# Performance work log

Hardware: AMD Instinct MI355X
Metric: run time of the kernel (lower is better)

The kernel has to match this reference:

```python
import jax, jax.numpy as jnp
import numpy as np

N_NODES = 50000


def setup_inputs() -> dict:
    key = jax.random.key(0)
    ks = jax.random.split(key, 12)
    node_features = jax.random.normal(ks[0], (50000, 256), dtype=jnp.float32)
    hedge_features = jax.random.normal(ks[1], (25000, 128), dtype=jnp.float32)
    node_senders = jax.random.randint(ks[2], (800000,), 0, 50000, dtype=jnp.int32)
    node_receivers = jnp.sort(jax.random.randint(ks[3], (800000,), 0, 50000, dtype=jnp.int32))
    node_convolution = jax.random.uniform(ks[4], (800000, 1), dtype=jnp.float32)
    hedge2node_senders = jax.random.randint(ks[5], (400000,), 0, 25000, dtype=jnp.int32)
    hedge2node_receivers = jnp.sort(jax.random.randint(ks[6], (400000,), 0, 50000, dtype=jnp.int32))
    hedge2node_convolution = jax.random.uniform(ks[7], (400000, 1), dtype=jnp.float32)
    # Linear params (flax convention: y = x @ W + b, W is [in, out])
    W_msg = jax.random.normal(ks[8], (256, 256), dtype=jnp.float32) / np.sqrt(256.0)
    b_msg = jax.random.normal(ks[9], (256,), dtype=jnp.float32) * 0.01
    W_scale = jax.random.normal(ks[10], (128, 256), dtype=jnp.float32) / np.sqrt(128.0)
    b_scale = jax.random.normal(ks[11], (256,), dtype=jnp.float32) * 0.01
    return {
        "node_features": node_features,
        "hedge_features": hedge_features,
        "node_senders": node_senders,
        "node_receivers": node_receivers,
        "node_convolution": node_convolution,
        "hedge2node_senders": hedge2node_senders,
        "hedge2node_receivers": hedge2node_receivers,
        "hedge2node_convolution": hedge2node_convolution,
        "W_msg": W_msg,
        "b_msg": b_msg,
        "W_scale": W_scale,
        "b_scale": b_scale,
    }


def reference(node_features, hedge_features, node_senders, node_receivers,
              node_convolution, hedge2node_senders, hedge2node_receivers,
              hedge2node_convolution, W_msg, b_msg, W_scale, b_scale):
    # node -> node message pipeline: gather, Linear, per-edge scale, segment_sum
    sender_features = node_features[node_senders]                     # [E, Fin]
    messages = sender_features @ W_msg + b_msg                        # [E, Fout]
    scaled_messages = node_convolution * messages                     # [E, Fout]
    gathered_messages = jax.ops.segment_sum(
        scaled_messages, node_receivers, num_segments=N_NODES)        # [N, Fout]
    # hedge -> node scaling pipeline: gather, Linear, per-edge scale, segment_sum
    hedge_sender_features = hedge_features[hedge2node_senders]        # [E2, Fh]
    hedge_messages = hedge_sender_features @ W_scale + b_scale        # [E2, Fout]
    scaled_hedge_messages = hedge2node_convolution * hedge_messages   # [E2, Fout]
    gathered_scaling = jax.ops.segment_sum(
        scaled_hedge_messages, hedge2node_receivers, num_segments=N_NODES)  # [N, Fout]
    # Hadamard combine
    return gathered_scaling * gathered_messages
```

## Files before the change

kernel.cpp:

```cpp
#include <hip/hip_runtime.h>


typedef __attribute__((ext_vector_type(8))) short bf16x8;
typedef __attribute__((ext_vector_type(4))) float f32x4;

static __device__ __forceinline__ unsigned short f2bf(float f) {
  unsigned u = __float_as_uint(f);
  u += 0x7fff + ((u >> 16) & 1);
  return (unsigned short)(u >> 16);
}
static __device__ __forceinline__ float bf2f(unsigned short h) {
  return __uint_as_float((unsigned)h << 16);
}

__global__ __launch_bounds__(256) void cvt_bf16(
    const float* __restrict__ src, unsigned short* __restrict__ dst, int n4)
{
  const int i = blockIdx.x * blockDim.x + threadIdx.x;
  if (i >= n4) return;
  const float4 v = reinterpret_cast<const float4*>(src)[i];
  reinterpret_cast<ushort4*>(dst)[i] =
      make_ushort4(f2bf(v.x), f2bf(v.y), f2bf(v.z), f2bf(v.w));
}

__global__ __launch_bounds__(256) void build_row_offsets(
    const int* __restrict__ rcv, int E, int N, int* __restrict__ row_start)
{
  const int e = blockIdx.x * blockDim.x + threadIdx.x;
  if (e >= E) return;
  const int c = rcv[e];
  const int p = (e == 0) ? -1 : rcv[e - 1];
  for (int n = p + 1; n <= c; ++n) row_start[n] = e;
  if (e == E - 1) {
    for (int n = c + 1; n <= N; ++n) row_start[n] = E;
  }
}

__global__ __launch_bounds__(256) void transpose_to_bf16(
    const float* __restrict__ W, unsigned short* __restrict__ WT, int K, int N)
{
  __shared__ float t[32][33];
  const int tx = threadIdx.x & 31, ty = threadIdx.x >> 5;
  const int n0 = blockIdx.x * 32, k0 = blockIdx.y * 32;
#pragma unroll
  for (int i = 0; i < 32; i += 8)
    t[ty + i][tx] = W[(size_t)(k0 + ty + i) * N + n0 + tx];
  __syncthreads();
#pragma unroll
  for (int i = 0; i < 32; i += 8)
    WT[(size_t)(n0 + ty + i) * K + k0 + tx] = f2bf(t[tx][ty + i]);
}

__global__ __launch_bounds__(256) void scatter_node_seg(
    const unsigned short* __restrict__ X,
    const int* __restrict__ snd,
    const float* __restrict__ conv,
    const int* __restrict__ row_start,
    unsigned short* __restrict__ A,
    float* __restrict__ csum,
    int N)
{
  const int lane = threadIdx.x & 63;
  const int node = __builtin_amdgcn_readfirstlane(
      (int)blockIdx.x * 4 + ((int)threadIdx.x >> 6));
  if (node >= N) return;
  const int lo = row_start[node];
  const int hi = row_start[node + 1];

  const unsigned short* Xl = X + lane * 4;
  float4 acc = make_float4(0.f, 0.f, 0.f, 0.f);
  float cacc = 0.f;

  int e = lo;
  for (; e + 8 <= hi; e += 8) {
    int s[8]; float cv[8]; ushort4 x[8];
#pragma unroll
    for (int j = 0; j < 8; ++j) s[j] = snd[e + j];
#pragma unroll
    for (int j = 0; j < 8; ++j) cv[j] = conv[e + j];
#pragma unroll
    for (int j = 0; j < 8; ++j)
      x[j] = *reinterpret_cast<const ushort4*>(Xl + (size_t)s[j] * 256);
#pragma unroll
    for (int j = 0; j < 8; ++j) {
      acc.x = fmaf(cv[j], bf2f(x[j].x), acc.x);
      acc.y = fmaf(cv[j], bf2f(x[j].y), acc.y);
      acc.z = fmaf(cv[j], bf2f(x[j].z), acc.z);
      acc.w = fmaf(cv[j], bf2f(x[j].w), acc.w);
      cacc += cv[j];
    }
  }
  for (; e < hi; ++e) {
    const int s = snd[e];
    const float cv = conv[e];
    const ushort4 x = *reinterpret_cast<const ushort4*>(Xl + (size_t)s * 256);
    acc.x = fmaf(cv, bf2f(x.x), acc.x);
    acc.y = fmaf(cv, bf2f(x.y), acc.y);
    acc.z = fmaf(cv, bf2f(x.z), acc.z);
    acc.w = fmaf(cv, bf2f(x.w), acc.w);
    cacc += cv;
  }

  *reinterpret_cast<ushort4*>(A + (size_t)node * 256 + lane * 4) =
      make_ushort4(f2bf(acc.x), f2bf(acc.y), f2bf(acc.z), f2bf(acc.w));
  if (lane == 0) csum[node] = cacc;
}

__global__ __launch_bounds__(256) void scatter_hedge_seg(
    const unsigned short* __restrict__ X,
    const int* __restrict__ snd,
    const float* __restrict__ conv,
    const int* __restrict__ row_start,
    unsigned short* __restrict__ B,
    float* __restrict__ csum,
    int N)
{
  const int lane = threadIdx.x & 63;
  const int node = __builtin_amdgcn_readfirstlane(
      (int)blockIdx.x * 4 + ((int)threadIdx.x >> 6));
  if (node >= N) return;
  const int lo = row_start[node];
  const int hi = row_start[node + 1];

  const unsigned short* Xl = X + lane * 2;
  float2 acc = make_float2(0.f, 0.f);
  float cacc = 0.f;

  int e = lo;
  for (; e + 8 <= hi; e += 8) {
    int s[8]; float cv[8]; ushort2 x[8];
#pragma unroll
    for (int j = 0; j < 8; ++j) s[j] = snd[e + j];
#pragma unroll
    for (int j = 0; j < 8; ++j) cv[j] = conv[e + j];
#pragma unroll
    for (int j = 0; j < 8; ++j)
      x[j] = *reinterpret_cast<const ushort2*>(Xl + (size_t)s[j] * 128);
#pragma unroll
    for (int j = 0; j < 8; ++j) {
      acc.x = fmaf(cv[j], bf2f(x[j].x), acc.x);
      acc.y = fmaf(cv[j], bf2f(x[j].y), acc.y);
      cacc += cv[j];
    }
  }
  for (; e < hi; ++e) {
    const int s = snd[e];
    const float cv = conv[e];
    const ushort2 x = *reinterpret_cast<const ushort2*>(Xl + (size_t)s * 128);
    acc.x = fmaf(cv, bf2f(x.x), acc.x);
    acc.y = fmaf(cv, bf2f(x.y), acc.y);
    cacc += cv;
  }

  *reinterpret_cast<ushort2*>(B + (size_t)node * 128 + lane * 2) =
      make_ushort2(f2bf(acc.x), f2bf(acc.y));
  if (lane == 0) csum[node] = cacc;
}

__global__ __launch_bounds__(512) void gemm_combine_mfma(
    const unsigned short* __restrict__ A,
    const unsigned short* __restrict__ B,
    const float* __restrict__ c1,
    const float* __restrict__ c2,
    const unsigned short* __restrict__ WmT,
    const float* __restrict__ bm,
    const unsigned short* __restrict__ WsT,
    const float* __restrict__ bs,
    float* __restrict__ out,
    int M)
{
  __shared__ unsigned short lWm[64][264];
  __shared__ unsigned short lWs[64][136];

  const int tid  = (int)threadIdx.x;
  const int lane = tid & 63;
  const int wv   = tid >> 6;
  const int l15  = lane & 15;
  const int lg   = lane >> 4;
  const int m0      = blockIdx.x * 256;
  const int colBlk  = blockIdx.y * 64;

  for (int i = tid; i < 64 * 256 / 8; i += 512) {
    const int c = i >> 5, k8 = (i & 31) << 3;
    *reinterpret_cast<bf16x8*>(&lWm[c][k8]) =
        *reinterpret_cast<const bf16x8*>(WmT + (size_t)(colBlk + c) * 256 + k8);
  }
  for (int i = tid; i < 64 * 128 / 8; i += 512) {
    const int c = i >> 4, k8 = (i & 15) << 3;
    *reinterpret_cast<bf16x8*>(&lWs[c][k8]) =
        *reinterpret_cast<const bf16x8*>(WsT + (size_t)(colBlk + c) * 128 + k8);
  }
  __syncthreads();

  const int rowA = m0 + wv * 32 + l15;

  f32x4 accM[2][4];
  f32x4 accS[2][4];
#pragma unroll
  for (int ms = 0; ms < 2; ++ms)
#pragma unroll
    for (int n = 0; n < 4; ++n) {
      accM[ms][n] = (f32x4)0.f;
      accS[ms][n] = (f32x4)0.f;
    }

#pragma unroll
  for (int kc = 0; kc < 256; kc += 32) {
    const int ko = kc + lg * 8;
    const bf16x8 a0 = *reinterpret_cast<const bf16x8*>(A + (size_t)rowA * 256 + ko);
    const bf16x8 a1 = *reinterpret_cast<const bf16x8*>(A + (size_t)(rowA + 16) * 256 + ko);
#pragma unroll
    for (int n = 0; n < 4; ++n) {
      const bf16x8 w = *reinterpret_cast<const bf16x8*>(&lWm[l15 + n * 16][ko]);
      accM[0][n] = __builtin_amdgcn_mfma_f32_16x16x32_bf16(a0, w, accM[0][n], 0, 0, 0);
      accM[1][n] = __builtin_amdgcn_mfma_f32_16x16x32_bf16(a1, w, accM[1][n], 0, 0, 0);
    }
  }

#pragma unroll
  for (int kc = 0; kc < 128; kc += 32) {
    const int ko = kc + lg * 8;
    const bf16x8 b0 = *reinterpret_cast<const bf16x8*>(B + (size_t)rowA * 128 + ko);
    const bf16x8 b1 = *reinterpret_cast<const bf16x8*>(B + (size_t)(rowA + 16) * 128 + ko);
#pragma unroll
    for (int n = 0; n < 4; ++n) {
      const bf16x8 w = *reinterpret_cast<const bf16x8*>(&lWs[l15 + n * 16][ko]);
      accS[0][n] = __builtin_amdgcn_mfma_f32_16x16x32_bf16(b0, w, accS[0][n], 0, 0, 0);
      accS[1][n] = __builtin_amdgcn_mfma_f32_16x16x32_bf16(b1, w, accS[1][n], 0, 0, 0);
    }
  }

  float bmv[4], bsv[4];
#pragma unroll
  for (int n = 0; n < 4; ++n) {
    bmv[n] = bm[colBlk + n * 16 + l15];
    bsv[n] = bs[colBlk + n * 16 + l15];
  }
#pragma unroll
  for (int ms = 0; ms < 2; ++ms) {
    const int rbase = m0 + wv * 32 + ms * 16 + lg * 4;
#pragma unroll
    for (int r = 0; r < 4; ++r) {
      const int row = rbase + r;
      if (row < M) {
        const float k1 = c1[row];
        const float k2 = c2[row];
#pragma unroll
        for (int n = 0; n < 4; ++n) {
          const int col = colBlk + n * 16 + l15;
          const float mv = accM[ms][n][r] + k1 * bmv[n];
          const float sv = accS[ms][n][r] + k2 * bsv[n];
          out[(size_t)row * 256 + col] = mv * sv;
        }
      }
    }
  }
}

extern "C" void kernel_launch(void* const* d_in, const int* in_sizes, int n_in,
                              void* d_out, int out_size, void* d_ws, size_t ws_size,
                              hipStream_t stream) {
  const float* node_features  = (const float*)d_in[0];
  const float* hedge_features = (const float*)d_in[1];
  const int*   node_senders   = (const int*)d_in[2];
  const int*   node_receivers = (const int*)d_in[3];
  const float* node_conv      = (const float*)d_in[4];
  const int*   h2n_senders    = (const int*)d_in[5];
  const int*   h2n_receivers  = (const int*)d_in[6];
  const float* h2n_conv       = (const float*)d_in[7];
  const float* Wm             = (const float*)d_in[8];
  const float* bm             = (const float*)d_in[9];
  const float* Ws             = (const float*)d_in[10];
  const float* bs             = (const float*)d_in[11];
  float* out = (float*)d_out;

  const int M   = in_sizes[0] / 256;
  const int Nh  = in_sizes[1] / 128;
  const int E   = in_sizes[2];
  const int E2  = in_sizes[5];
  const int Mp  = ((M + 255) / 256) * 256;

  unsigned short* Ab  = (unsigned short*)d_ws;
  unsigned short* Bb  = Ab + (size_t)Mp * 256;
  unsigned short* Xb  = Bb + (size_t)Mp * 128;
  unsigned short* Hb  = Xb + (size_t)M * 256;
  unsigned short* WmT = Hb + (size_t)Nh * 128;
  unsigned short* WsT = WmT + 256 * 256;
  float* c1 = (float*)(WsT + 256 * 128);
  float* c2 = c1 + Mp;
  int*   ro1 = (int*)(c2 + Mp);
  int*   ro2 = ro1 + (M + 1);

  const int nx4 = M * 256 / 4, nh4 = Nh * 128 / 4;
  cvt_bf16<<<(nx4 + 255) / 256, 256, 0, stream>>>(node_features, Xb, nx4);
  cvt_bf16<<<(nh4 + 255) / 256, 256, 0, stream>>>(hedge_features, Hb, nh4);

  build_row_offsets<<<(E + 255) / 256, 256, 0, stream>>>(
      node_receivers, E, M, ro1);
  build_row_offsets<<<(E2 + 255) / 256, 256, 0, stream>>>(
      h2n_receivers, E2, M, ro2);

  transpose_to_bf16<<<dim3(256 / 32, 256 / 32), 256, 0, stream>>>(
      Wm, WmT, 256, 256);
  transpose_to_bf16<<<dim3(256 / 32, 128 / 32), 256, 0, stream>>>(
      Ws, WsT, 128, 256);

  scatter_node_seg<<<(M + 3) / 4, 256, 0, stream>>>(
      Xb, node_senders, node_conv, ro1, Ab, c1, M);
  scatter_hedge_seg<<<(M + 3) / 4, 256, 0, stream>>>(
      Hb, h2n_senders, h2n_conv, ro2, Bb, c2, M);

  gemm_combine_mfma<<<dim3(Mp / 256, 4), 512, 0, stream>>>(
      Ab, Bb, c1, c2, WmT, bm, WsT, bs, out, M);
}
```

Before: 145.0 us.

## Merge prep kernels into one launch and fuse both segment scatters

The six preprocessing launches (bf16 conversions, row-offset builds, weight transposes) become a single kernel that dispatches on block index. The node and hedge segment-gather kernels are likewise merged into one grid, so both can run at the same time. The node path's unroll goes from 8 to 16 edges, with a 4-wide middle loop. The aim is to cut per-launch overhead and tail idle time between small kernels, at the cost of more register pressure in the fused gather kernel.

```diff
diff --git a/kernel.cpp b/kernel.cpp
--- a/kernel.cpp
+++ b/kernel.cpp
@@ -13,148 +13,209 @@
   return __uint_as_float((unsigned)h << 16);
 }
 
-__global__ __launch_bounds__(256) void cvt_bf16(
-    const float* __restrict__ src, unsigned short* __restrict__ dst, int n4)
-{
-  const int i = blockIdx.x * blockDim.x + threadIdx.x;
-  if (i >= n4) return;
-  const float4 v = reinterpret_cast<const float4*>(src)[i];
-  reinterpret_cast<ushort4*>(dst)[i] =
-      make_ushort4(f2bf(v.x), f2bf(v.y), f2bf(v.z), f2bf(v.w));
-}
-
-__global__ __launch_bounds__(256) void build_row_offsets(
-    const int* __restrict__ rcv, int E, int N, int* __restrict__ row_start)
-{
-  const int e = blockIdx.x * blockDim.x + threadIdx.x;
-  if (e >= E) return;
-  const int c = rcv[e];
-  const int p = (e == 0) ? -1 : rcv[e - 1];
-  for (int n = p + 1; n <= c; ++n) row_start[n] = e;
-  if (e == E - 1) {
-    for (int n = c + 1; n <= N; ++n) row_start[n] = E;
-  }
-}
-
-__global__ __launch_bounds__(256) void transpose_to_bf16(
-    const float* __restrict__ W, unsigned short* __restrict__ WT, int K, int N)
+__global__ __launch_bounds__(256) void prep_all(
+    const float* __restrict__ X, const float* __restrict__ H,
+    const int* __restrict__ rcv1, int E1,
+    const int* __restrict__ rcv2, int E2, int N,
+    const float* __restrict__ Wm, const float* __restrict__ Ws,
+    unsigned short* __restrict__ Xb, unsigned short* __restrict__ Hb,
+    int* __restrict__ ro1, int* __restrict__ ro2,
+    unsigned short* __restrict__ WmT, unsigned short* __restrict__ WsT,
+    int nX4, int nH4)
 {
   __shared__ float t[32][33];
-  const int tx = threadIdx.x & 31, ty = threadIdx.x >> 5;
-  const int n0 = blockIdx.x * 32, k0 = blockIdx.y * 32;
-#pragma unroll
-  for (int i = 0; i < 32; i += 8)
-    t[ty + i][tx] = W[(size_t)(k0 + ty + i) * N + n0 + tx];
-  __syncthreads();
-#pragma unroll
-  for (int i = 0; i < 32; i += 8)
-    WT[(size_t)(n0 + ty + i) * K + k0 + tx] = f2bf(t[tx][ty + i]);
-}
-
-__global__ __launch_bounds__(256) void scatter_node_seg(
+  const int tid = (int)threadIdx.x;
+  int b = (int)blockIdx.x;
+
+  const int bX  = (nX4 + 255) / 256;
+  const int bH  = (nH4 + 255) / 256;
+  const int bE1 = (E1 + 255) / 256;
+  const int bE2 = (E2 + 255) / 256;
+
+  if (b < bX) {
+    const int i = b * 256 + tid;
+    if (i < nX4) {
+      const float4 v = reinterpret_cast<const float4*>(X)[i];
+      reinterpret_cast<ushort4*>(Xb)[i] =
+          make_ushort4(f2bf(v.x), f2bf(v.y), f2bf(v.z), f2bf(v.w));
+    }
+    return;
+  }
+  b -= bX;
+  if (b < bH) {
+    const int i = b * 256 + tid;
+    if (i < nH4) {
+      const float4 v = reinterpret_cast<const float4*>(H)[i];
+      reinterpret_cast<ushort4*>(Hb)[i] =
+          make_ushort4(f2bf(v.x), f2bf(v.y), f2bf(v.z), f2bf(v.w));
+    }
+    return;
+  }
+  b -= bH;
+  if (b < bE1) {
+    const int e = b * 256 + tid;
+    if (e < E1) {
+      const int c = rcv1[e];
+      const int p = (e == 0) ? -1 : rcv1[e - 1];
+      for (int n = p + 1; n <= c; ++n) ro1[n] = e;
+      if (e == E1 - 1)
+        for (int n = c + 1; n <= N; ++n) ro1[n] = E1;
+    }
+    return;
+  }
+  b -= bE1;
+  if (b < bE2) {
+    const int e = b * 256 + tid;
+    if (e < E2) {
+      const int c = rcv2[e];
+      const int p = (e == 0) ? -1 : rcv2[e - 1];
+      for (int n = p + 1; n <= c; ++n) ro2[n] = e;
+      if (e == E2 - 1)
+        for (int n = c + 1; n <= N; ++n) ro2[n] = E2;
+    }
+    return;
+  }
+  b -= bE2;
+  {
+    const float* W; unsigned short* WT; int K, Nn, tile;
+    if (b < 64) { W = Wm; WT = WmT; K = 256; Nn = 256; tile = b; }
+    else        { W = Ws; WT = WsT; K = 128; Nn = 256; tile = b - 64; }
+    const int ntiles_n = Nn / 32;
+    const int n0 = (tile % ntiles_n) * 32;
+    const int k0 = (tile / ntiles_n) * 32;
+    const int tx = tid & 31, ty = tid >> 5;
+#pragma unroll
+    for (int i = 0; i < 32; i += 8)
+      t[ty + i][tx] = W[(size_t)(k0 + ty + i) * Nn + n0 + tx];
+    __syncthreads();
+#pragma unroll
+    for (int i = 0; i < 32; i += 8)
+      WT[(size_t)(n0 + ty + i) * K + k0 + tx] = f2bf(t[tx][ty + i]);
+  }
+}
+
+__global__ __launch_bounds__(256) void scatter_fused(
     const unsigned short* __restrict__ X,
-    const int* __restrict__ snd,
-    const float* __restrict__ conv,
-    const int* __restrict__ row_start,
+    const int* __restrict__ snd1,
+    const float* __restrict__ conv1,
+    const int* __restrict__ ro1,
     unsigned short* __restrict__ A,
-    float* __restrict__ csum,
+    float* __restrict__ c1,
+    const unsigned short* __restrict__ Hf,
+    const int* __restrict__ snd2,
+    const float* __restrict__ conv2,
+    const int* __restrict__ ro2,
+    unsigned short* __restrict__ B,
+    float* __restrict__ c2,
     int N)
 {
   const int lane = threadIdx.x & 63;
-  const int node = __builtin_amdgcn_readfirstlane(
-      (int)blockIdx.x * 4 + ((int)threadIdx.x >> 6));
-  if (node >= N) return;
-  const int lo = row_start[node];
-  const int hi = row_start[node + 1];
-
-  const unsigned short* Xl = X + lane * 4;
-  float4 acc = make_float4(0.f, 0.f, 0.f, 0.f);
-  float cacc = 0.f;
-
-  int e = lo;
-  for (; e + 8 <= hi; e += 8) {
-    int s[8]; float cv[8]; ushort4 x[8];
-#pragma unroll
-    for (int j = 0; j < 8; ++j) s[j] = snd[e + j];
-#pragma unroll
-    for (int j = 0; j < 8; ++j) cv[j] = conv[e + j];
-#pragma unroll
-    for (int j = 0; j < 8; ++j)
-      x[j] = *reinterpret_cast<const ushort4*>(Xl + (size_t)s[j] * 256);
-#pragma unroll
-    for (int j = 0; j < 8; ++j) {
-      acc.x = fmaf(cv[j], bf2f(x[j].x), acc.x);
-      acc.y = fmaf(cv[j], bf2f(x[j].y), acc.y);
-      acc.z = fmaf(cv[j], bf2f(x[j].z), acc.z);
-      acc.w = fmaf(cv[j], bf2f(x[j].w), acc.w);
-      cacc += cv[j];
-    }
-  }
-  for (; e < hi; ++e) {
-    const int s = snd[e];
-    const float cv = conv[e];
-    const ushort4 x = *reinterpret_cast<const ushort4*>(Xl + (size_t)s * 256);
-    acc.x = fmaf(cv, bf2f(x.x), acc.x);
-    acc.y = fmaf(cv, bf2f(x.y), acc.y);
-    acc.z = fmaf(cv, bf2f(x.z), acc.z);
-    acc.w = fmaf(cv, bf2f(x.w), acc.w);
-    cacc += cv;
-  }
-
-  *reinterpret_cast<ushort4*>(A + (size_t)node * 256 + lane * 4) =
-      make_ushort4(f2bf(acc.x), f2bf(acc.y), f2bf(acc.z), f2bf(acc.w));
-  if (lane == 0) csum[node] = cacc;
-}
-
-__global__ __launch_bounds__(256) void scatter_hedge_seg(
-    const unsigned short* __restrict__ X,
-    const int* __restrict__ snd,
-    const float* __restrict__ conv,
-    const int* __restrict__ row_start,
-    unsigned short* __restrict__ B,
-    float* __restrict__ csum,
-    int N)
-{
-  const int lane = threadIdx.x & 63;
-  const int node = __builtin_amdgcn_readfirstlane(
-      (int)blockIdx.x * 4 + ((int)threadIdx.x >> 6));
-  if (node >= N) return;
-  const int lo = row_start[node];
-  const int hi = row_start[node + 1];
-
-  const unsigned short* Xl = X + lane * 2;
-  float2 acc = make_float2(0.f, 0.f);
-  float cacc = 0.f;
-
-  int e = lo;
-  for (; e + 8 <= hi; e += 8) {
-    int s[8]; float cv[8]; ushort2 x[8];
-#pragma unroll
-    for (int j = 0; j < 8; ++j) s[j] = snd[e + j];
-#pragma unroll
-    for (int j = 0; j < 8; ++j) cv[j] = conv[e + j];
-#pragma unroll
-    for (int j = 0; j < 8; ++j)
-      x[j] = *reinterpret_cast<const ushort2*>(Xl + (size_t)s[j] * 128);
-#pragma unroll
-    for (int j = 0; j < 8; ++j) {
-      acc.x = fmaf(cv[j], bf2f(x[j].x), acc.x);
-      acc.y = fmaf(cv[j], bf2f(x[j].y), acc.y);
-      cacc += cv[j];
-    }
-  }
-  for (; e < hi; ++e) {
-    const int s = snd[e];
-    const float cv = conv[e];
-    const ushort2 x = *reinterpret_cast<const ushort2*>(Xl + (size_t)s * 128);
-    acc.x = fmaf(cv, bf2f(x.x), acc.x);
-    acc.y = fmaf(cv, bf2f(x.y), acc.y);
-    cacc += cv;
-  }
-
-  *reinterpret_cast<ushort2*>(B + (size_t)node * 128 + lane * 2) =
-      make_ushort2(f2bf(acc.x), f2bf(acc.y));
-  if (lane == 0) csum[node] = cacc;
+  const int bNode = (N + 3) / 4;
+  const int bid = (int)blockIdx.x;
+
+  if (bid < bNode) {
+    const int node = __builtin_amdgcn_readfirstlane(
+        bid * 4 + ((int)threadIdx.x >> 6));
+    if (node >= N) return;
+    const int lo = ro1[node];
+    const int hi = ro1[node + 1];
+
+    const unsigned short* Xl = X + lane * 4;
+    float4 acc = make_float4(0.f, 0.f, 0.f, 0.f);
+    float cacc = 0.f;
+
+    int e = lo;
+    for (; e + 16 <= hi; e += 16) {
+      int s[16]; float cv[16]; ushort4 x[16];
+#pragma unroll
+      for (int j = 0; j < 16; ++j) s[j] = snd1[e + j];
+#pragma unroll
+      for (int j = 0; j < 16; ++j) cv[j] = conv1[e + j];
+#pragma unroll
+      for (int j = 0; j < 16; ++j)
+        x[j] = *reinterpret_cast<const ushort4*>(Xl + (size_t)s[j] * 256);
+#pragma unroll
+      for (int j = 0; j < 16; ++j) {
+        acc.x = fmaf(cv[j], bf2f(x[j].x), acc.x);
+        acc.y = fmaf(cv[j], bf2f(x[j].y), acc.y);
+        acc.z = fmaf(cv[j], bf2f(x[j].z), acc.z);
+        acc.w = fmaf(cv[j], bf2f(x[j].w), acc.w);
+        cacc += cv[j];
+      }
+    }
+    for (; e + 4 <= hi; e += 4) {
+      int s[4]; float cv[4]; ushort4 x[4];
+#pragma unroll
+      for (int j = 0; j < 4; ++j) s[j] = snd1[e + j];
+#pragma unroll
+      for (int j = 0; j < 4; ++j) cv[j] = conv1[e + j];
+#pragma unroll
+      for (int j = 0; j < 4; ++j)
+        x[j] = *reinterpret_cast<const ushort4*>(Xl + (size_t)s[j] * 256);
+#pragma unroll
+      for (int j = 0; j < 4; ++j) {
+        acc.x = fmaf(cv[j], bf2f(x[j].x), acc.x);
+        acc.y = fmaf(cv[j], bf2f(x[j].y), acc.y);
+        acc.z = fmaf(cv[j], bf2f(x[j].z), acc.z);
+        acc.w = fmaf(cv[j], bf2f(x[j].w), acc.w);
+        cacc += cv[j];
+      }
+    }
+    for (; e < hi; ++e) {
+      const int s = snd1[e];
+      const float cv = conv1[e];
+      const ushort4 x = *reinterpret_cast<const ushort4*>(Xl + (size_t)s * 256);
+      acc.x = fmaf(cv, bf2f(x.x), acc.x);
+      acc.y = fmaf(cv, bf2f(x.y), acc.y);
+      acc.z = fmaf(cv, bf2f(x.z), acc.z);
+      acc.w = fmaf(cv, bf2f(x.w), acc.w);
+      cacc += cv;
+    }
+
+    *reinterpret_cast<ushort4*>(A + (size_t)node * 256 + lane * 4) =
+        make_ushort4(f2bf(acc.x), f2bf(acc.y), f2bf(acc.z), f2bf(acc.w));
+    if (lane == 0) c1[node] = cacc;
+  } else {
+    const int node = __builtin_amdgcn_readfirstlane(
+        (bid - bNode) * 4 + ((int)threadIdx.x >> 6));
+    if (node >= N) return;
+    const int lo = ro2[node];
+    const int hi = ro2[node + 1];
+
+    const unsigned short* Hl = Hf + lane * 2;
+    float2 acc = make_float2(0.f, 0.f);
+    float cacc = 0.f;
+
+    int e = lo;
+    for (; e + 8 <= hi; e += 8) {
+      int s[8]; float cv[8]; ushort2 x[8];
+#pragma unroll
+      for (int j = 0; j < 8; ++j) s[j] = snd2[e + j];
+#pragma unroll
+      for (int j = 0; j < 8; ++j) cv[j] = conv2[e + j];
+#pragma unroll
+      for (int j = 0; j < 8; ++j)
+        x[j] = *reinterpret_cast<const ushort2*>(Hl + (size_t)s[j] * 128);
+#pragma unroll
+      for (int j = 0; j < 8; ++j) {
+        acc.x = fmaf(cv[j], bf2f(x[j].x), acc.x);
+        acc.y = fmaf(cv[j], bf2f(x[j].y), acc.y);
+        cacc += cv[j];
+      }
+    }
+    for (; e < hi; ++e) {
+      const int s = snd2[e];
+      const float cv = conv2[e];
+      const ushort2 x = *reinterpret_cast<const ushort2*>(Hl + (size_t)s * 128);
+      acc.x = fmaf(cv, bf2f(x.x), acc.x);
+      acc.y = fmaf(cv, bf2f(x.y), acc.y);
+      cacc += cv;
+    }
+
+    *reinterpret_cast<ushort2*>(B + (size_t)node * 128 + lane * 2) =
+        make_ushort2(f2bf(acc.x), f2bf(acc.y));
+    if (lane == 0) c2[node] = cacc;
+  }
 }
 
 __global__ __launch_bounds__(512) void gemm_combine_mfma(
@@ -291,23 +352,21 @@
   int*   ro1 = (int*)(c2 + Mp);
   int*   ro2 = ro1 + (M + 1);
 
-  const int nx4 = M * 256 / 4, nh4 = Nh * 128 / 4;
-  cvt_bf16<<<(nx4 + 255) / 256, 256, 0, stream>>>(node_features, Xb, nx4);
-  cvt_bf16<<<(nh4 + 255) / 256, 256, 0, stream>>>(hedge_features, Hb, nh4);
-
-  build_row_offsets<<<(E + 255) / 256, 256, 0, stream>>>(
-      node_receivers, E, M, ro1);
-  build_row_offsets<<<(E2 + 255) / 256, 256, 0, stream>>>(
-      h2n_receivers, E2, M, ro2);
-
-  transpose_to_bf16<<<dim3(256 / 32, 256 / 32), 256, 0, stream>>>(
-      Wm, WmT, 256, 256);
-  transpose_to_bf16<<<dim3(256 / 32, 128 / 32), 256, 0, stream>>>(
-      Ws, WsT, 128, 256);
-
-  scatter_node_seg<<<(M + 3) / 4, 256, 0, stream>>>(
-      Xb, node_senders, node_conv, ro1, Ab, c1, M);
-  scatter_hedge_seg<<<(M + 3) / 4, 256, 0, stream>>>(
+  const int nX4 = M * 256 / 4, nH4 = Nh * 128 / 4;
+  const int bX  = (nX4 + 255) / 256;
+  const int bH  = (nH4 + 255) / 256;
+  const int bE1 = (E + 255) / 256;
+  const int bE2 = (E2 + 255) / 256;
+  const int prep_blocks = bX + bH + bE1 + bE2 + 64 + 32;
+
+  prep_all<<<prep_blocks, 256, 0, stream>>>(
+      node_features, hedge_features,
+      node_receivers, E, h2n_receivers, E2, M,
+      Wm, Ws, Xb, Hb, ro1, ro2, WmT, WsT, nX4, nH4);
+
+  const int bNode = (M + 3) / 4;
+  scatter_fused<<<bNode * 2, 256, 0, stream>>>(
+      Xb, node_senders, node_conv, ro1, Ab, c1,
       Hb, h2n_senders, h2n_conv, ro2, Bb, c2, M);
 
   gemm_combine_mfma<<<dim3(Mp / 256, 4), 512, 0, stream>>>(
```

Result: faster. 134.3 us (-7.4%).
